# Optimization experiments

Hardware: AMD Instinct MI355X
Metric: run time of the kernel (lower is better)

## Reference

```python
import jax, jax.numpy as jnp
import numpy as np

# Dimensions per init_kwargs / input_specs
B, N, C = 8192, 4, 2048          # tokens, expansion_rate, hidden_dim
SINKHORN_ITERS = 20
EPS = 1e-5
ALPHA_INIT = 0.01


def setup_inputs() -> dict:
    key = jax.random.key(0)
    k1, k2 = jax.random.split(key)
    return {
        "x_expanded": jax.random.normal(k1, (B, N, C), dtype=jnp.float32),
        "rmsnorm_weight": jnp.ones((C,), dtype=jnp.float32),   # init: ones
        "H_pre": jnp.zeros((N,), dtype=jnp.float32),            # init: zeros
        "H_post": jnp.zeros((N,), dtype=jnp.float32),           # init: zeros
        "H_res": ALPHA_INIT * jax.random.normal(k2, (N, N), dtype=jnp.float32),
    }


def _sinkhorn(M, iters, eps):
    """Iterative row/column normalization -> (approximately) doubly-stochastic."""
    def body(_, M):
        M = M / (jnp.sum(M, axis=1, keepdims=True) + eps)  # row normalize
        M = M / (jnp.sum(M, axis=0, keepdims=True) + eps)  # col normalize
        return M
    return jax.lax.fori_loop(0, iters, body, M)


def reference(x_expanded, rmsnorm_weight, H_pre, H_post, H_res):
    # RMSNorm over hidden dim C, per (token, branch)
    ms = jnp.mean(x_expanded * x_expanded, axis=-1, keepdims=True)  # [B, N, 1]
    x_norm = x_expanded * jax.lax.rsqrt(ms + EPS) * rmsnorm_weight  # [B, N, C]

    # Manifold-constrained residual mixing matrix (doubly stochastic via Sinkhorn)
    H = _sinkhorn(jnp.exp(H_res), SINKHORN_ITERS, EPS)              # [N, N]

    pre = jax.nn.sigmoid(H_pre)    # [N] input-aggregation weights
    post = jax.nn.sigmoid(H_post)  # [N] output-distribution weights

    # Aggregate normalized branches into a single stream, redistribute,
    # and add the Sinkhorn-mixed residual of the raw branches.
    x_agg = jnp.einsum('n,bnc->bc', pre, x_norm)                     # [B, C]
    y = jnp.einsum('mn,bnc->bmc', H, x_expanded) \
        + post[None, :, None] * x_agg[:, None, :]                    # [B, N, C]
    return y
```

## Files before the change

kernel.cpp:

```cpp
#include <hip/hip_runtime.h>
#include <math.h>

#define B_TOK 8192
#define NB 4
#define CH 2048
#define TPB 512
#define NBLK 1024
#define TOK_PER_BLK 8
#define SINK_ITERS 20
#define EPS 1e-5f

typedef float f32x4 __attribute__((ext_vector_type(4)));

__global__ void mhc_sinkhorn(const float* __restrict__ H_pre,
                             const float* __restrict__ H_post,
                             const float* __restrict__ H_res,
                             float* __restrict__ ws)
{
    if (threadIdx.x == 0) {
        float M[NB][NB];
        #pragma unroll
        for (int i = 0; i < NB; ++i)
            #pragma unroll
            for (int j = 0; j < NB; ++j)
                M[i][j] = expf(H_res[i * NB + j]);

        for (int it = 0; it < SINK_ITERS; ++it) {
            #pragma unroll
            for (int i = 0; i < NB; ++i) {
                float r = 1.0f / (M[i][0] + M[i][1] + M[i][2] + M[i][3] + EPS);
                #pragma unroll
                for (int j = 0; j < NB; ++j) M[i][j] *= r;
            }
            #pragma unroll
            for (int j = 0; j < NB; ++j) {
                float r = 1.0f / (M[0][j] + M[1][j] + M[2][j] + M[3][j] + EPS);
                #pragma unroll
                for (int i = 0; i < NB; ++i) M[i][j] *= r;
            }
        }
        #pragma unroll
        for (int i = 0; i < NB; ++i)
            #pragma unroll
            for (int j = 0; j < NB; ++j)
                ws[i * NB + j] = M[i][j];
        #pragma unroll
        for (int n = 0; n < NB; ++n) {
            ws[16 + n] = 1.0f / (1.0f + expf(-H_pre[n]));
            ws[20 + n] = 1.0f / (1.0f + expf(-H_post[n]));
        }
    }
}

__global__ __launch_bounds__(TPB) void mhc_main(const float* __restrict__ x,
                                                const float* __restrict__ w,
                                                const float* __restrict__ ws,
                                                float* __restrict__ y)
{
    const int t = threadIdx.x;
    const int wave = t >> 6;
    const int lane = t & 63;

    const float H00 = ws[0],  H01 = ws[1],  H02 = ws[2],  H03 = ws[3];
    const float H10 = ws[4],  H11 = ws[5],  H12 = ws[6],  H13 = ws[7];
    const float H20 = ws[8],  H21 = ws[9],  H22 = ws[10], H23 = ws[11];
    const float H30 = ws[12], H31 = ws[13], H32 = ws[14], H33 = ws[15];
    const float pre0 = ws[16], pre1 = ws[17], pre2 = ws[18], pre3 = ws[19];
    const float ps0  = ws[20], ps1  = ws[21], ps2  = ws[22], ps3  = ws[23];

    __shared__ f32x4 red4[2][TPB / 64];

    const f32x4 wv = ((const f32x4*)w)[t];
    const int b0 = blockIdx.x * TOK_PER_BLK;

    auto xload = [&](int b, f32x4& d0, f32x4& d1, f32x4& d2, f32x4& d3) {
        const f32x4* p = (const f32x4*)x + (size_t)b * (NB * CH / 4) + t;
        d0 = __builtin_nontemporal_load(p);
        d1 = __builtin_nontemporal_load(p + (CH / 4));
        d2 = __builtin_nontemporal_load(p + 2 * (CH / 4));
        d3 = __builtin_nontemporal_load(p + 3 * (CH / 4));
    };

    auto process = [&](int b, f32x4 x0, f32x4 x1, f32x4 x2, f32x4 x3, int ph) {
        float s0 = x0.x * x0.x + x0.y * x0.y + x0.z * x0.z + x0.w * x0.w;
        float s1 = x1.x * x1.x + x1.y * x1.y + x1.z * x1.z + x1.w * x1.w;
        float s2 = x2.x * x2.x + x2.y * x2.y + x2.z * x2.z + x2.w * x2.w;
        float s3 = x3.x * x3.x + x3.y * x3.y + x3.z * x3.z + x3.w * x3.w;
        #pragma unroll
        for (int m = 1; m < 64; m <<= 1) {
            s0 += __shfl_xor(s0, m);
            s1 += __shfl_xor(s1, m);
            s2 += __shfl_xor(s2, m);
            s3 += __shfl_xor(s3, m);
        }
        if (lane == 0) {
            f32x4 v = { s0, s1, s2, s3 };
            red4[ph][wave] = v;
        }

        __builtin_amdgcn_sched_barrier(0);
        asm volatile("s_waitcnt lgkmcnt(0)" ::: "memory");
        __builtin_amdgcn_s_barrier();
        __builtin_amdgcn_sched_barrier(0);

        f32x4 r0 = red4[ph][0], r1 = red4[ph][1], r2 = red4[ph][2], r3 = red4[ph][3];
        f32x4 r4 = red4[ph][4], r5 = red4[ph][5], r6 = red4[ph][6], r7 = red4[ph][7];
        float t0 = ((r0.x + r1.x) + (r2.x + r3.x)) + ((r4.x + r5.x) + (r6.x + r7.x));
        float t1 = ((r0.y + r1.y) + (r2.y + r3.y)) + ((r4.y + r5.y) + (r6.y + r7.y));
        float t2 = ((r0.z + r1.z) + (r2.z + r3.z)) + ((r4.z + r5.z) + (r6.z + r7.z));
        float t3 = ((r0.w + r1.w) + (r2.w + r3.w)) + ((r4.w + r5.w) + (r6.w + r7.w));

        const float a0 = pre0 * rsqrtf(t0 * (1.0f / CH) + EPS);
        const float a1 = pre1 * rsqrtf(t1 * (1.0f / CH) + EPS);
        const float a2 = pre2 * rsqrtf(t2 * (1.0f / CH) + EPS);
        const float a3 = pre3 * rsqrtf(t3 * (1.0f / CH) + EPS);

        f32x4 wu;
        wu.x = wv.x * (a0 * x0.x + a1 * x1.x + a2 * x2.x + a3 * x3.x);
        wu.y = wv.y * (a0 * x0.y + a1 * x1.y + a2 * x2.y + a3 * x3.y);
        wu.z = wv.z * (a0 * x0.z + a1 * x1.z + a2 * x2.z + a3 * x3.z);
        wu.w = wv.w * (a0 * x0.w + a1 * x1.w + a2 * x2.w + a3 * x3.w);

        f32x4* yp = (f32x4*)y + (size_t)b * (NB * CH / 4) + t;
        f32x4 o;
        o.x = H00 * x0.x + H01 * x1.x + H02 * x2.x + H03 * x3.x + ps0 * wu.x;
        o.y = H00 * x0.y + H01 * x1.y + H02 * x2.y + H03 * x3.y + ps0 * wu.y;
        o.z = H00 * x0.z + H01 * x1.z + H02 * x2.z + H03 * x3.z + ps0 * wu.z;
        o.w = H00 * x0.w + H01 * x1.w + H02 * x2.w + H03 * x3.w + ps0 * wu.w;
        __builtin_nontemporal_store(o, yp);
        o.x = H10 * x0.x + H11 * x1.x + H12 * x2.x + H13 * x3.x + ps1 * wu.x;
        o.y = H10 * x0.y + H11 * x1.y + H12 * x2.y + H13 * x3.y + ps1 * wu.y;
        o.z = H10 * x0.z + H11 * x1.z + H12 * x2.z + H13 * x3.z + ps1 * wu.z;
        o.w = H10 * x0.w + H11 * x1.w + H12 * x2.w + H13 * x3.w + ps1 * wu.w;
        __builtin_nontemporal_store(o, yp + (CH / 4));
        o.x = H20 * x0.x + H21 * x1.x + H22 * x2.x + H23 * x3.x + ps2 * wu.x;
        o.y = H20 * x0.y + H21 * x1.y + H22 * x2.y + H23 * x3.y + ps2 * wu.y;
        o.z = H20 * x0.z + H21 * x1.z + H22 * x2.z + H23 * x3.z + ps2 * wu.z;
        o.w = H20 * x0.w + H21 * x1.w + H22 * x2.w + H23 * x3.w + ps2 * wu.w;
        __builtin_nontemporal_store(o, yp + 2 * (CH / 4));
        o.x = H30 * x0.x + H31 * x1.x + H32 * x2.x + H33 * x3.x + ps3 * wu.x;
        o.y = H30 * x0.y + H31 * x1.y + H32 * x2.y + H33 * x3.y + ps3 * wu.y;
        o.z = H30 * x0.z + H31 * x1.z + H32 * x2.z + H33 * x3.z + ps3 * wu.z;
        o.w = H30 * x0.w + H31 * x1.w + H32 * x2.w + H33 * x3.w + ps3 * wu.w;
        __builtin_nontemporal_store(o, yp + 3 * (CH / 4));
    };

    f32x4 xA0, xA1, xA2, xA3, xB0, xB1, xB2, xB3;

    xload(b0 + 0, xA0, xA1, xA2, xA3);
    xload(b0 + 1, xB0, xB1, xB2, xB3);
    process(b0 + 0, xA0, xA1, xA2, xA3, 0);
    xload(b0 + 2, xA0, xA1, xA2, xA3);
    process(b0 + 1, xB0, xB1, xB2, xB3, 1);
    xload(b0 + 3, xB0, xB1, xB2, xB3);
    process(b0 + 2, xA0, xA1, xA2, xA3, 0);
    xload(b0 + 4, xA0, xA1, xA2, xA3);
    process(b0 + 3, xB0, xB1, xB2, xB3, 1);
    xload(b0 + 5, xB0, xB1, xB2, xB3);
    process(b0 + 4, xA0, xA1, xA2, xA3, 0);
    xload(b0 + 6, xA0, xA1, xA2, xA3);
    process(b0 + 5, xB0, xB1, xB2, xB3, 1);
    xload(b0 + 7, xB0, xB1, xB2, xB3);
    process(b0 + 6, xA0, xA1, xA2, xA3, 0);
    process(b0 + 7, xB0, xB1, xB2, xB3, 1);
}

extern "C" void kernel_launch(void* const* d_in, const int* in_sizes, int n_in,
                              void* d_out, int out_size, void* d_ws, size_t ws_size,
                              hipStream_t stream) {
    const float* x      = (const float*)d_in[0];
    const float* wgt    = (const float*)d_in[1];
    const float* h_pre  = (const float*)d_in[2];
    const float* h_post = (const float*)d_in[3];
    const float* h_res  = (const float*)d_in[4];
    float* y  = (float*)d_out;
    float* ws = (float*)d_ws;

    mhc_sinkhorn<<<1, 64, 0, stream>>>(h_pre, h_post, h_res, ws);
    mhc_main<<<NBLK, TPB, 0, stream>>>(x, wgt, ws, y);
}
```

Before: 108.2 us.

## Fuse Sinkhorn setup into main kernel with wave-parallel shuffle normalization

Removes the separate single-thread Sinkhorn launch and has every wave recompute the 4x4 matrix redundantly, using 16 lanes with xor-shuffles for the row and column sums, then broadcasting the entries via readlane. The first two token loads are issued before this computation so the redundant work overlaps memory latency. This saves a kernel launch and the inter-kernel dependency gap, at the cost of extra per-wave ALU work and the use of an approximate reciprocal instead of an exact divide.

```diff
diff --git a/kernel.cpp b/kernel.cpp
--- a/kernel.cpp
+++ b/kernel.cpp
@@ -12,67 +12,29 @@
 
 typedef float f32x4 __attribute__((ext_vector_type(4)));
 
-__global__ void mhc_sinkhorn(const float* __restrict__ H_pre,
-                             const float* __restrict__ H_post,
-                             const float* __restrict__ H_res,
-                             float* __restrict__ ws)
-{
-    if (threadIdx.x == 0) {
-        float M[NB][NB];
-        #pragma unroll
-        for (int i = 0; i < NB; ++i)
-            #pragma unroll
-            for (int j = 0; j < NB; ++j)
-                M[i][j] = expf(H_res[i * NB + j]);
-
-        for (int it = 0; it < SINK_ITERS; ++it) {
-            #pragma unroll
-            for (int i = 0; i < NB; ++i) {
-                float r = 1.0f / (M[i][0] + M[i][1] + M[i][2] + M[i][3] + EPS);
-                #pragma unroll
-                for (int j = 0; j < NB; ++j) M[i][j] *= r;
-            }
-            #pragma unroll
-            for (int j = 0; j < NB; ++j) {
-                float r = 1.0f / (M[0][j] + M[1][j] + M[2][j] + M[3][j] + EPS);
-                #pragma unroll
-                for (int i = 0; i < NB; ++i) M[i][j] *= r;
-            }
-        }
-        #pragma unroll
-        for (int i = 0; i < NB; ++i)
-            #pragma unroll
-            for (int j = 0; j < NB; ++j)
-                ws[i * NB + j] = M[i][j];
-        #pragma unroll
-        for (int n = 0; n < NB; ++n) {
-            ws[16 + n] = 1.0f / (1.0f + expf(-H_pre[n]));
-            ws[20 + n] = 1.0f / (1.0f + expf(-H_post[n]));
-        }
-    }
+__device__ __forceinline__ float bcast_first(float v) {
+    return __uint_as_float(__builtin_amdgcn_readfirstlane(__float_as_uint(v)));
+}
+__device__ __forceinline__ float read_lane(float v, int l) {
+    return __uint_as_float(__builtin_amdgcn_readlane(__float_as_uint(v), l));
 }
 
-__global__ __launch_bounds__(TPB) void mhc_main(const float* __restrict__ x,
-                                                const float* __restrict__ w,
-                                                const float* __restrict__ ws,
-                                                float* __restrict__ y)
+__global__ __launch_bounds__(TPB) void mhc_fused(
+    const float* __restrict__ x,
+    const float* __restrict__ w,
+    const float* __restrict__ H_pre,
+    const float* __restrict__ H_post,
+    const float* __restrict__ H_res,
+    float* __restrict__ y)
 {
     const int t = threadIdx.x;
     const int wave = t >> 6;
     const int lane = t & 63;
-
-    const float H00 = ws[0],  H01 = ws[1],  H02 = ws[2],  H03 = ws[3];
-    const float H10 = ws[4],  H11 = ws[5],  H12 = ws[6],  H13 = ws[7];
-    const float H20 = ws[8],  H21 = ws[9],  H22 = ws[10], H23 = ws[11];
-    const float H30 = ws[12], H31 = ws[13], H32 = ws[14], H33 = ws[15];
-    const float pre0 = ws[16], pre1 = ws[17], pre2 = ws[18], pre3 = ws[19];
-    const float ps0  = ws[20], ps1  = ws[21], ps2  = ws[22], ps3  = ws[23];
+    const int b0 = blockIdx.x * TOK_PER_BLK;
 
     __shared__ f32x4 red4[2][TPB / 64];
 
-    const f32x4 wv = ((const f32x4*)w)[t];
-    const int b0 = blockIdx.x * TOK_PER_BLK;
-
+    f32x4 xA0, xA1, xA2, xA3, xB0, xB1, xB2, xB3;
     auto xload = [&](int b, f32x4& d0, f32x4& d1, f32x4& d2, f32x4& d3) {
         const f32x4* p = (const f32x4*)x + (size_t)b * (NB * CH / 4) + t;
         d0 = __builtin_nontemporal_load(p);
@@ -80,6 +42,38 @@
         d2 = __builtin_nontemporal_load(p + 2 * (CH / 4));
         d3 = __builtin_nontemporal_load(p + 3 * (CH / 4));
     };
+    xload(b0 + 0, xA0, xA1, xA2, xA3);
+    xload(b0 + 1, xB0, xB1, xB2, xB3);
+    const f32x4 wv = ((const f32x4*)w)[t];
+
+    const int e = lane & 15;
+    float v = expf(H_res[e]);
+    #pragma unroll 1
+    for (int it = 0; it < SINK_ITERS; ++it) {
+        float s = v + __shfl_xor(v, 1);
+        s += __shfl_xor(s, 2);
+        v *= __builtin_amdgcn_rcpf(s + EPS);
+        s = v + __shfl_xor(v, 4);
+        s += __shfl_xor(s, 8);
+        v *= __builtin_amdgcn_rcpf(s + EPS);
+    }
+    const float H00 = read_lane(v, 0),  H01 = read_lane(v, 1),
+                H02 = read_lane(v, 2),  H03 = read_lane(v, 3);
+    const float H10 = read_lane(v, 4),  H11 = read_lane(v, 5),
+                H12 = read_lane(v, 6),  H13 = read_lane(v, 7);
+    const float H20 = read_lane(v, 8),  H21 = read_lane(v, 9),
+                H22 = read_lane(v, 10), H23 = read_lane(v, 11);
+    const float H30 = read_lane(v, 12), H31 = read_lane(v, 13),
+                H32 = read_lane(v, 14), H33 = read_lane(v, 15);
+
+    const float pre0 = bcast_first(1.0f / (1.0f + expf(-H_pre[0])));
+    const float pre1 = bcast_first(1.0f / (1.0f + expf(-H_pre[1])));
+    const float pre2 = bcast_first(1.0f / (1.0f + expf(-H_pre[2])));
+    const float pre3 = bcast_first(1.0f / (1.0f + expf(-H_pre[3])));
+    const float ps0  = bcast_first(1.0f / (1.0f + expf(-H_post[0])));
+    const float ps1  = bcast_first(1.0f / (1.0f + expf(-H_post[1])));
+    const float ps2  = bcast_first(1.0f / (1.0f + expf(-H_post[2])));
+    const float ps3  = bcast_first(1.0f / (1.0f + expf(-H_post[3])));
 
     auto process = [&](int b, f32x4 x0, f32x4 x1, f32x4 x2, f32x4 x3, int ph) {
         float s0 = x0.x * x0.x + x0.y * x0.y + x0.z * x0.z + x0.w * x0.w;
@@ -94,8 +88,8 @@
             s3 += __shfl_xor(s3, m);
         }
         if (lane == 0) {
-            f32x4 v = { s0, s1, s2, s3 };
-            red4[ph][wave] = v;
+            f32x4 pv = { s0, s1, s2, s3 };
+            red4[ph][wave] = pv;
         }
 
         __builtin_amdgcn_sched_barrier(0);
@@ -145,10 +139,6 @@
         __builtin_nontemporal_store(o, yp + 3 * (CH / 4));
     };
 
-    f32x4 xA0, xA1, xA2, xA3, xB0, xB1, xB2, xB3;
-
-    xload(b0 + 0, xA0, xA1, xA2, xA3);
-    xload(b0 + 1, xB0, xB1, xB2, xB3);
     process(b0 + 0, xA0, xA1, xA2, xA3, 0);
     xload(b0 + 2, xA0, xA1, xA2, xA3);
     process(b0 + 1, xB0, xB1, xB2, xB3, 1);
@@ -173,9 +163,7 @@
     const float* h_pre  = (const float*)d_in[2];
     const float* h_post = (const float*)d_in[3];
     const float* h_res  = (const float*)d_in[4];
-    float* y  = (float*)d_out;
-    float* ws = (float*)d_ws;
+    float* y = (float*)d_out;
 
-    mhc_sinkhorn<<<1, 64, 0, stream>>>(h_pre, h_post, h_res, ws);
-    mhc_main<<<NBLK, TPB, 0, stream>>>(x, wgt, ws, y);
+    mhc_fused<<<NBLK, TPB, 0, stream>>>(x, wgt, h_pre, h_post, h_res, y);
 }
```

New measurement: 102.4 us. 5.3% less time.
